# Kernel tuning notes

Hardware: AMD Instinct MI355X
Metric: run time of the kernel (lower is better)

Reference implementation:

```python
import jax, jax.numpy as jnp
import numpy as np

B, H, W, C = 16, 56, 56, 256
NH, WS, SS = 8, 7, 3            # heads, window size, shift size
N = WS * WS                     # tokens per window (49)
NW = (H // WS) * (W // WS)      # windows per image (64)
HID = 4 * C                     # mlp hidden
SCALE = (C // NH) ** -0.5
EPS = 1e-5


def _rel_pos_index():
    coords = np.stack(np.meshgrid(np.arange(WS), np.arange(WS), indexing='ij'))  # (2,WS,WS)
    cf = coords.reshape(2, -1)
    rel = (cf[:, :, None] - cf[:, None, :]).transpose(1, 2, 0).copy()  # (N,N,2)
    rel[:, :, 0] += WS - 1
    rel[:, :, 1] += WS - 1
    rel[:, :, 0] *= 2 * WS - 1
    return rel.sum(-1).reshape(-1)  # (N*N,)

REL_IDX = jnp.asarray(_rel_pos_index())


def _attn_mask():
    # Swin SW-MSA mask for the cyclic shift
    img = np.zeros((H, W), np.float32)
    cnt = 0
    for hs in (slice(0, -WS), slice(-WS, -SS), slice(-SS, None)):
        for ws_ in (slice(0, -WS), slice(-WS, -SS), slice(-SS, None)):
            img[hs, ws_] = cnt
            cnt += 1
    mw = img.reshape(H // WS, WS, W // WS, WS).transpose(0, 2, 1, 3).reshape(-1, N)
    am = mw[:, None, :] - mw[:, :, None]
    return np.where(am != 0, -100.0, 0.0).astype(np.float32)  # (NW,N,N)


def layernorm(x, g, b):
    mu = x.mean(-1, keepdims=True)
    var = jnp.mean((x - mu) ** 2, axis=-1, keepdims=True)
    return (x - mu) * jax.lax.rsqrt(var + EPS) * g + b


def window_partition(x):  # (B,H,W,C) -> (B*NW,N,C)
    b = x.shape[0]
    x = x.reshape(b, H // WS, WS, W // WS, WS, C).transpose(0, 1, 3, 2, 4, 5)
    return x.reshape(-1, N, C)


def window_reverse(w):  # (B*NW,N,C) -> (B,H,W,C)
    x = w.reshape(-1, H // WS, W // WS, WS, WS, C).transpose(0, 1, 3, 2, 4, 5)
    return x.reshape(-1, H, W, C)


def setup_inputs() -> dict:
    key = jax.random.key(0)
    ks = jax.random.split(key, 16)
    sd = 0.02
    return {
        'x': jax.random.normal(ks[0], (B, H * W, C), jnp.float32),
        'w_qkv': jax.random.normal(ks[1], (C, 3 * C), jnp.float32) * sd,
        'b_qkv': jnp.zeros((3 * C,), jnp.float32),
        'rel_bias': jax.random.normal(ks[2], ((2 * WS - 1) ** 2, NH), jnp.float32) * sd,
        'w_proj': jax.random.normal(ks[3], (C, C), jnp.float32) * sd,
        'b_proj': jnp.zeros((C,), jnp.float32),
        'g1': jnp.ones((C,), jnp.float32),
        'beta1': jnp.zeros((C,), jnp.float32),
        'g2': jnp.ones((C,), jnp.float32),
        'beta2': jnp.zeros((C,), jnp.float32),
        'w_fc1': jax.random.normal(ks[4], (C, HID), jnp.float32) * sd,
        'b_fc1': jnp.zeros((HID,), jnp.float32),
        'w_fc2': jax.random.normal(ks[5], (HID, C), jnp.float32) * sd,
        'b_fc2': jnp.zeros((C,), jnp.float32),
        'attn_mask': jnp.asarray(_attn_mask()),
    }


def reference(x, w_qkv, b_qkv, rel_bias, w_proj, b_proj, g1, beta1, g2, beta2,
              w_fc1, b_fc1, w_fc2, b_fc2, attn_mask):
    shortcut = x
    xn = layernorm(x, g1, beta1).reshape(B, H, W, C)
    # cyclic shift (shift_size > 0 path)
    xs = jnp.roll(xn, shift=(-SS, -SS), axis=(1, 2))
    xw = window_partition(xs)                                   # (B*NW, N, C)
    qkv = (xw @ w_qkv + b_qkv).reshape(-1, N, 3, NH, C // NH)
    q, k, v = [jnp.transpose(qkv[:, :, i], (0, 2, 1, 3)) for i in range(3)]  # (Bw,NH,N,hd)
    attn = jnp.einsum('whnd,whmd->whnm', q * SCALE, k)          # (Bw,NH,N,N)
    rpb = rel_bias[REL_IDX].reshape(N, N, NH).transpose(2, 0, 1)  # (NH,N,N)
    attn = attn + rpb[None]
    attn = attn.reshape(B, NW, NH, N, N) + attn_mask[None, :, None]
    attn = jax.nn.softmax(attn.reshape(-1, NH, N, N), axis=-1)
    out = jnp.einsum('whnm,whmd->whnd', attn, v)                # (Bw,NH,N,hd)
    out = out.transpose(0, 2, 1, 3).reshape(-1, N, C)
    out = out @ w_proj + b_proj
    xs = window_reverse(out)                                    # (B,H,W,C)
    xr = jnp.roll(xs, shift=(SS, SS), axis=(1, 2)).reshape(B, H * W, C)
    x = shortcut + xr
    h = layernorm(x, g2, beta2)
    h = jax.nn.gelu(h @ w_fc1 + b_fc1, approximate=False) @ w_fc2 + b_fc2
    return x + h
```

## Files before the change

kernel.cpp:

```cpp
#include <hip/hip_runtime.h>
#include <hip/hip_bf16.h>

typedef unsigned short u16;
typedef __bf16 bf16x8 __attribute__((ext_vector_type(8)));
typedef float f32x4 __attribute__((ext_vector_type(4)));
typedef unsigned int u32x4 __attribute__((ext_vector_type(4)));

#define SCALE_F 0.17677669529663687f

__device__ __forceinline__ u16 f2b(float f) {
    unsigned u = __builtin_bit_cast(unsigned, f);
    u = (u + 0x7fffu + ((u >> 16) & 1u)) >> 16;
    return (u16)u;
}

__device__ __forceinline__ f32x4 mfma16(bf16x8 a, bf16x8 b, f32x4 c) {
    return __builtin_amdgcn_mfma_f32_16x16x32_bf16(a, b, c, 0, 0, 0);
}

__global__ __launch_bounds__(256)
void prep_kernel(const float* __restrict__ wqkv, const float* __restrict__ wproj,
                 const float* __restrict__ wfc1, const float* __restrict__ wfc2,
                 const float* __restrict__ relb, const float* __restrict__ amask,
                 u16* __restrict__ wqkvT, u16* __restrict__ wprojT,
                 u16* __restrict__ wfc1T, u16* __restrict__ wfc2T,
                 float* __restrict__ bm)
{
    int idx = blockIdx.x * 256 + threadIdx.x;
    if (idx < 196608) { int n = idx >> 8, k = idx & 255; wqkvT[idx] = f2b(wqkv[k*768 + n]); return; }
    idx -= 196608;
    if (idx < 65536)  { int n = idx >> 8, k = idx & 255; wprojT[idx] = f2b(wproj[k*256 + n]); return; }
    idx -= 65536;
    if (idx < 262144) { int n = idx >> 8, k = idx & 255; wfc1T[idx] = f2b(wfc1[k*1024 + n]); return; }
    idx -= 262144;
    if (idx < 262144) { int n = idx >> 10, k = idx & 1023; wfc2T[idx] = f2b(wfc2[k*256 + n]); return; }
    idx -= 262144;
    int m = idx & 63, t = idx >> 6;
    int n = t & 63; t >>= 6;
    int h = t & 7;  t >>= 3;
    float v = -1e30f;
    if (n < 49 && m < 49) {
        int iq = n / 7, jq = n - iq * 7, ik = m / 7, jk = m - ik * 7;
        int rel = (iq - ik + 6) * 13 + (jq - jk + 6);
        v = relb[rel * 8 + h] + amask[(t * 49 + n) * 49 + m];
    }
    bm[idx] = v;
}

__global__ __launch_bounds__(256)
void ln_kernel(const float* __restrict__ x, const float* __restrict__ g,
               const float* __restrict__ be, u16* __restrict__ out, const int mode)
{
    const int wid  = ((blockIdx.x << 8) + threadIdx.x) >> 6;
    const int lane = threadIdx.x & 63;
    size_t srcoff;
    if (mode == 0) {
        int bw = wid / 49, nt = wid - bw * 49;
        int b = bw >> 6, widx = bw & 63;
        int wh = widx >> 3, ww = widx & 7;
        int ti = nt / 7, tj = nt - ti * 7;
        int hh = wh * 7 + ti + 3; if (hh >= 56) hh -= 56;
        int wp = ww * 7 + tj + 3; if (wp >= 56) wp -= 56;
        srcoff = ((size_t)b * 3136 + hh * 56 + wp) << 8;
    } else {
        srcoff = (size_t)wid << 8;
    }
    float4 v = *(const float4*)(x + srcoff + (lane << 2));
    float s  = v.x + v.y + v.z + v.w;
    float s2 = fmaf(v.x, v.x, fmaf(v.y, v.y, fmaf(v.z, v.z, v.w * v.w)));
    #pragma unroll
    for (int k = 1; k < 64; k <<= 1) { s += __shfl_xor(s, k); s2 += __shfl_xor(s2, k); }
    const float mu   = s * 0.00390625f;
    const float rstd = rsqrtf(s2 * 0.00390625f - mu * mu + 1e-5f);
    float4 gv = *(const float4*)(g  + (lane << 2));
    float4 bv = *(const float4*)(be + (lane << 2));
    ushort4 o;
    o.x = f2b((v.x - mu) * rstd * gv.x + bv.x);
    o.y = f2b((v.y - mu) * rstd * gv.y + bv.y);
    o.z = f2b((v.z - mu) * rstd * gv.z + bv.z);
    o.w = f2b((v.w - mu) * rstd * gv.w + bv.w);
    *(ushort4*)(out + ((size_t)wid << 8) + (lane << 2)) = o;
}

template<int MODE>
__global__ __launch_bounds__(256)
void gemm128(const u16* __restrict__ A, const u16* __restrict__ Bt,
             const float* __restrict__ bias, void* __restrict__ Cout,
             const int N, const int K, const float* __restrict__ resid)
{
    constexpr int LDA = 40;
    __shared__ __align__(16) u16 As[128 * LDA];
    __shared__ __align__(16) u16 Bs[128 * LDA];

    const int tid  = threadIdx.x;
    const int wave = tid >> 6, lane = tid & 63;
    const int q = lane >> 4, l15 = lane & 15;
    const int wm = wave >> 1, wn = wave & 1;
    const int m0 = blockIdx.y << 7, n0 = blockIdx.x << 7;

    f32x4 acc[4][4] = {};

    const int ar = tid >> 2;
    const int ac = (tid & 3) << 3;
    const u16* Ag = A  + (size_t)(m0 + ar) * K + ac;
    const u16* Bg = Bt + (size_t)(n0 + ar) * K + ac;
    const size_t rstep = (size_t)64 * K;

    u32x4 ra0 = *(const u32x4*)Ag;
    u32x4 ra1 = *(const u32x4*)(Ag + rstep);
    u32x4 rb0 = *(const u32x4*)Bg;
    u32x4 rb1 = *(const u32x4*)(Bg + rstep);

    const int KT = K >> 5;
    for (int kt = 0; kt < KT; ++kt) {
        __syncthreads();
        *(u32x4*)&As[ar * LDA + ac]        = ra0;
        *(u32x4*)&As[(ar + 64) * LDA + ac] = ra1;
        *(u32x4*)&Bs[ar * LDA + ac]        = rb0;
        *(u32x4*)&Bs[(ar + 64) * LDA + ac] = rb1;
        if (kt + 1 < KT) {
            const u16* Ag2 = Ag + (kt + 1) * 32;
            const u16* Bg2 = Bg + (kt + 1) * 32;
            ra0 = *(const u32x4*)Ag2;
            ra1 = *(const u32x4*)(Ag2 + rstep);
            rb0 = *(const u32x4*)Bg2;
            rb1 = *(const u32x4*)(Bg2 + rstep);
        }
        __syncthreads();
        bf16x8 af[4], bfv[4];
        #pragma unroll
        for (int i = 0; i < 4; ++i)
            af[i] = *(const bf16x8*)&As[(wm * 64 + i * 16 + l15) * LDA + q * 8];
        #pragma unroll
        for (int j = 0; j < 4; ++j)
            bfv[j] = *(const bf16x8*)&Bs[(wn * 64 + j * 16 + l15) * LDA + q * 8];
        #pragma unroll
        for (int i = 0; i < 4; ++i)
            #pragma unroll
            for (int j = 0; j < 4; ++j)
                acc[i][j] = mfma16(af[i], bfv[j], acc[i][j]);
    }

    #pragma unroll
    for (int i = 0; i < 4; ++i) {
        #pragma unroll
        for (int r = 0; r < 4; ++r) {
            const int m = m0 + wm * 64 + i * 16 + q * 4 + r;
            size_t dstrow = 0;
            if (MODE == 1) {
                int bw = m / 49, nt = m - bw * 49;
                int b = bw >> 6, widx = bw & 63;
                int wh = widx >> 3, ww2 = widx & 7;
                int ti = nt / 7, tj = nt - ti * 7;
                int hh = wh * 7 + ti + 3;  if (hh >= 56) hh -= 56;
                int wp = ww2 * 7 + tj + 3; if (wp >= 56) wp -= 56;
                dstrow = ((size_t)b * 3136 + hh * 56 + wp) << 8;
            }
            #pragma unroll
            for (int j = 0; j < 4; ++j) {
                const int col = n0 + wn * 64 + j * 16 + l15;
                float v = acc[i][j][r] + bias[col];
                if (MODE == 0) {
                    ((u16*)Cout)[(size_t)m * N + col] = f2b(v);
                } else if (MODE == 2) {
                    float y = 0.7978845608028654f * (v + 0.044715f * v * v * v);
                    float t = __expf(2.0f * y);
                    float rr = __builtin_amdgcn_rcpf(t + 1.0f);
                    v = v - v * rr;
                    ((u16*)Cout)[(size_t)m * N + col] = f2b(v);
                } else if (MODE == 3) {
                    const size_t o = (size_t)m * N + col;
                    ((float*)Cout)[o] = resid[o] + v;
                } else {
                    const size_t o = dstrow + col;
                    ((float*)Cout)[o] = resid[o] + v;
                }
            }
        }
    }
}

__global__ __launch_bounds__(64)
void attn_kernel(const u16* __restrict__ qkv, const float* __restrict__ bm,
                 u16* __restrict__ out)
{
    constexpr int LDP = 72;
    __shared__ __align__(16) u16 Pl[64 * LDP];
    __shared__ __align__(16) u16 Vt[32 * LDP];

    const int bw   = blockIdx.x >> 3;
    const int h    = blockIdx.x & 7;
    const int widx = bw & 63;
    const int lane = threadIdx.x;
    const int q = lane >> 4, l15 = lane & 15;

    const u16* base = qkv + (size_t)bw * 49 * 768 + h * 32;

    {
        const int key = lane;
        const u16* vp = base + 512 + (size_t)(key < 49 ? key : 0) * 768;
        __align__(16) u16 tmp[32];
        #pragma unroll
        for (int c = 0; c < 4; ++c)
            *(u32x4*)&tmp[c * 8] = *(const u32x4*)(vp + c * 8);
        #pragma unroll
        for (int d = 0; d < 32; ++d)
            Vt[d * LDP + key] = (key < 49) ? tmp[d] : (u16)0;
    }

    bf16x8 aq[4], bk[4];
    #pragma unroll
    for (int i = 0; i < 4; ++i) {
        int row = i * 16 + l15; row = (row < 49) ? row : 0;
        aq[i] = *(const bf16x8*)(base + (size_t)row * 768 + q * 8);
    }
    #pragma unroll
    for (int j = 0; j < 4; ++j) {
        int key = j * 16 + l15; key = (key < 49) ? key : 0;
        bk[j] = *(const bf16x8*)(base + (size_t)key * 768 + 256 + q * 8);
    }
    f32x4 s[4][4];
    #pragma unroll
    for (int i = 0; i < 4; ++i)
        #pragma unroll
        for (int j = 0; j < 4; ++j) {
            f32x4 z = {0.f, 0.f, 0.f, 0.f};
            s[i][j] = mfma16(aq[i], bk[j], z);
        }

    const float* bmb = bm + ((size_t)(widx * 8 + h) << 12);
    #pragma unroll
    for (int i = 0; i < 4; ++i) {
        #pragma unroll
        for (int r = 0; r < 4; ++r) {
            const int n = i * 16 + q * 4 + r;
            const float* rowp = bmb + (n << 6) + l15;
            #pragma unroll
            for (int j = 0; j < 4; ++j)
                s[i][j][r] = fmaf(s[i][j][r], SCALE_F, rowp[j * 16]);
        }
    }

    #pragma unroll
    for (int i = 0; i < 4; ++i) {
        #pragma unroll
        for (int r = 0; r < 4; ++r) {
            float mx = fmaxf(fmaxf(s[i][0][r], s[i][1][r]), fmaxf(s[i][2][r], s[i][3][r]));
            #pragma unroll
            for (int k = 1; k < 16; k <<= 1) mx = fmaxf(mx, __shfl_xor(mx, k));
            float p[4], sum = 0.f;
            #pragma unroll
            for (int j = 0; j < 4; ++j) { p[j] = __expf(s[i][j][r] - mx); sum += p[j]; }
            #pragma unroll
            for (int k = 1; k < 16; k <<= 1) sum += __shfl_xor(sum, k);
            const float inv = 1.0f / sum;
            const int n = i * 16 + q * 4 + r;
            #pragma unroll
            for (int j = 0; j < 4; ++j)
                Pl[n * LDP + j * 16 + l15] = f2b(p[j] * inv);
        }
    }
    __syncthreads();

    f32x4 o[4][2] = {};
    #pragma unroll
    for (int ks = 0; ks < 2; ++ks) {
        bf16x8 ap[4], bv[2];
        #pragma unroll
        for (int i = 0; i < 4; ++i)
            ap[i] = *(const bf16x8*)&Pl[(i * 16 + l15) * LDP + ks * 32 + q * 8];
        #pragma unroll
        for (int jd = 0; jd < 2; ++jd)
            bv[jd] = *(const bf16x8*)&Vt[(jd * 16 + l15) * LDP + ks * 32 + q * 8];
        #pragma unroll
        for (int i = 0; i < 4; ++i)
            #pragma unroll
            for (int jd = 0; jd < 2; ++jd)
                o[i][jd] = mfma16(ap[i], bv[jd], o[i][jd]);
    }

    #pragma unroll
    for (int i = 0; i < 4; ++i) {
        #pragma unroll
        for (int r = 0; r < 4; ++r) {
            const int n = i * 16 + q * 4 + r;
            if (n < 49) {
                u16* op = out + ((size_t)(bw * 49 + n) << 8) + h * 32;
                #pragma unroll
                for (int jd = 0; jd < 2; ++jd)
                    op[jd * 16 + l15] = f2b(o[i][jd][r]);
            }
        }
    }
}

extern "C" void kernel_launch(void* const* d_in, const int* in_sizes, int n_in,
                              void* d_out, int out_size, void* d_ws, size_t ws_size,
                              hipStream_t stream) {
    const float* x      = (const float*)d_in[0];
    const float* w_qkv  = (const float*)d_in[1];
    const float* b_qkv  = (const float*)d_in[2];
    const float* rel_b  = (const float*)d_in[3];
    const float* w_proj = (const float*)d_in[4];
    const float* b_proj = (const float*)d_in[5];
    const float* g1     = (const float*)d_in[6];
    const float* be1    = (const float*)d_in[7];
    const float* g2     = (const float*)d_in[8];
    const float* be2    = (const float*)d_in[9];
    const float* w_fc1  = (const float*)d_in[10];
    const float* b_fc1  = (const float*)d_in[11];
    const float* w_fc2  = (const float*)d_in[12];
    const float* b_fc2  = (const float*)d_in[13];
    const float* amask  = (const float*)d_in[14];

    char* ws = (char*)d_ws;
    u16*   xw     = (u16*)(ws);
    u16*   qkvb   = (u16*)(ws + 25690112);
    u16*   attno  = (u16*)(ws + 102760448);
    float* x2     = (float*)(ws + 128450560);
    u16*   wqkvT  = (u16*)(ws + 179830784);
    u16*   wprojT = (u16*)(ws + 180224000);
    u16*   wfc1T  = (u16*)(ws + 180355072);
    u16*   wfc2T  = (u16*)(ws + 180879360);
    float* bm     = (float*)(ws + 181403648);
    u16*   h1     = qkvb;

    prep_kernel<<<12288, 256, 0, stream>>>(w_qkv, w_proj, w_fc1, w_fc2, rel_b, amask,
                                           wqkvT, wprojT, wfc1T, wfc2T, bm);
    ln_kernel<<<12544, 256, 0, stream>>>(x, g1, be1, xw, 0);
    gemm128<0><<<dim3(6, 392), 256, 0, stream>>>(xw, wqkvT, b_qkv, qkvb, 768, 256, nullptr);
    attn_kernel<<<8192, 64, 0, stream>>>(qkvb, bm, attno);
    gemm128<1><<<dim3(2, 392), 256, 0, stream>>>(attno, wprojT, b_proj, x2, 256, 256, x);
    ln_kernel<<<12544, 256, 0, stream>>>(x2, g2, be2, xw, 1);
    gemm128<2><<<dim3(8, 392), 256, 0, stream>>>(xw, wfc1T, b_fc1, h1, 1024, 256, nullptr);
    gemm128<3><<<dim3(2, 392), 256, 0, stream>>>(h1, wfc2T, b_fc2, (float*)d_out, 256, 1024, x2);
}
```

Baseline: 375.4 us.

## Store residual intermediate in bf16 and remap GEMM blocks for XCD locality

The post-attention residual x2 is now stored as bf16 rather than fp32. It is written by the proj GEMM, read by the second layernorm and read as the residual in the fc2 GEMM, which halves that traffic. GEMM launches switch to a 1D grid whose block index is remapped so that consecutive row blocks land on the same XCD, aiming to improve L2 reuse of A tiles across column blocks. The trade-off is bf16 rounding in the residual stream, which adds accuracy error.

```diff
diff --git a/kernel.cpp b/kernel.cpp
--- a/kernel.cpp
+++ b/kernel.cpp
@@ -12,6 +12,10 @@
     unsigned u = __builtin_bit_cast(unsigned, f);
     u = (u + 0x7fffu + ((u >> 16) & 1u)) >> 16;
     return (u16)u;
+}
+__device__ __forceinline__ float b2f(u16 b) {
+    unsigned u = ((unsigned)b) << 16;
+    return __builtin_bit_cast(float, u);
 }
 
 __device__ __forceinline__ f32x4 mfma16(bf16x8 a, bf16x8 b, f32x4 c) {
@@ -48,12 +52,13 @@
 }
 
 __global__ __launch_bounds__(256)
-void ln_kernel(const float* __restrict__ x, const float* __restrict__ g,
-               const float* __restrict__ be, u16* __restrict__ out, const int mode)
+void ln_kernel(const float* __restrict__ x, const u16* __restrict__ xb,
+               const float* __restrict__ g, const float* __restrict__ be,
+               u16* __restrict__ out, const int mode)
 {
     const int wid  = ((blockIdx.x << 8) + threadIdx.x) >> 6;
     const int lane = threadIdx.x & 63;
-    size_t srcoff;
+    float4 v;
     if (mode == 0) {
         int bw = wid / 49, nt = wid - bw * 49;
         int b = bw >> 6, widx = bw & 63;
@@ -61,11 +66,12 @@
         int ti = nt / 7, tj = nt - ti * 7;
         int hh = wh * 7 + ti + 3; if (hh >= 56) hh -= 56;
         int wp = ww * 7 + tj + 3; if (wp >= 56) wp -= 56;
-        srcoff = ((size_t)b * 3136 + hh * 56 + wp) << 8;
+        size_t srcoff = ((size_t)b * 3136 + hh * 56 + wp) << 8;
+        v = *(const float4*)(x + srcoff + (lane << 2));
     } else {
-        srcoff = (size_t)wid << 8;
-    }
-    float4 v = *(const float4*)(x + srcoff + (lane << 2));
+        ushort4 raw = *(const ushort4*)(xb + ((size_t)wid << 8) + (lane << 2));
+        v.x = b2f(raw.x); v.y = b2f(raw.y); v.z = b2f(raw.z); v.w = b2f(raw.w);
+    }
     float s  = v.x + v.y + v.z + v.w;
     float s2 = fmaf(v.x, v.x, fmaf(v.y, v.y, fmaf(v.z, v.z, v.w * v.w)));
     #pragma unroll
@@ -86,7 +92,8 @@
 __global__ __launch_bounds__(256)
 void gemm128(const u16* __restrict__ A, const u16* __restrict__ Bt,
              const float* __restrict__ bias, void* __restrict__ Cout,
-             const int N, const int K, const float* __restrict__ resid)
+             const int N, const int K, const void* __restrict__ resid,
+             const int NB)
 {
     constexpr int LDA = 40;
     __shared__ __align__(16) u16 As[128 * LDA];
@@ -96,7 +103,13 @@
     const int wave = tid >> 6, lane = tid & 63;
     const int q = lane >> 4, l15 = lane & 15;
     const int wm = wave >> 1, wn = wave & 1;
-    const int m0 = blockIdx.y << 7, n0 = blockIdx.x << 7;
+
+    const int bid  = blockIdx.x;
+    const int xcd  = bid & 7;
+    const int t    = bid >> 3;
+    const int colb = t % NB;
+    const int rowb = xcd + ((t / NB) << 3);
+    const int m0 = rowb << 7, n0 = colb << 7;
 
     f32x4 acc[4][4] = {};
 
@@ -164,16 +177,16 @@
                     ((u16*)Cout)[(size_t)m * N + col] = f2b(v);
                 } else if (MODE == 2) {
                     float y = 0.7978845608028654f * (v + 0.044715f * v * v * v);
-                    float t = __expf(2.0f * y);
-                    float rr = __builtin_amdgcn_rcpf(t + 1.0f);
+                    float tt = __expf(2.0f * y);
+                    float rr = __builtin_amdgcn_rcpf(tt + 1.0f);
                     v = v - v * rr;
                     ((u16*)Cout)[(size_t)m * N + col] = f2b(v);
                 } else if (MODE == 3) {
                     const size_t o = (size_t)m * N + col;
-                    ((float*)Cout)[o] = resid[o] + v;
+                    ((float*)Cout)[o] = b2f(((const u16*)resid)[o]) + v;
                 } else {
                     const size_t o = dstrow + col;
-                    ((float*)Cout)[o] = resid[o] + v;
+                    ((u16*)Cout)[o] = f2b(((const float*)resid)[o] + v);
                 }
             }
         }
@@ -317,21 +330,21 @@
     u16*   xw     = (u16*)(ws);
     u16*   qkvb   = (u16*)(ws + 25690112);
     u16*   attno  = (u16*)(ws + 102760448);
-    float* x2     = (float*)(ws + 128450560);
-    u16*   wqkvT  = (u16*)(ws + 179830784);
-    u16*   wprojT = (u16*)(ws + 180224000);
-    u16*   wfc1T  = (u16*)(ws + 180355072);
-    u16*   wfc2T  = (u16*)(ws + 180879360);
-    float* bm     = (float*)(ws + 181403648);
+    u16*   x2b    = (u16*)(ws + 128450560);
+    u16*   wqkvT  = (u16*)(ws + 154140672);
+    u16*   wprojT = (u16*)(ws + 154533888);
+    u16*   wfc1T  = (u16*)(ws + 154664960);
+    u16*   wfc2T  = (u16*)(ws + 155189248);
+    float* bm     = (float*)(ws + 155713536);
     u16*   h1     = qkvb;
 
     prep_kernel<<<12288, 256, 0, stream>>>(w_qkv, w_proj, w_fc1, w_fc2, rel_b, amask,
                                            wqkvT, wprojT, wfc1T, wfc2T, bm);
-    ln_kernel<<<12544, 256, 0, stream>>>(x, g1, be1, xw, 0);
-    gemm128<0><<<dim3(6, 392), 256, 0, stream>>>(xw, wqkvT, b_qkv, qkvb, 768, 256, nullptr);
+    ln_kernel<<<12544, 256, 0, stream>>>(x, nullptr, g1, be1, xw, 0);
+    gemm128<0><<<392 * 6, 256, 0, stream>>>(xw, wqkvT, b_qkv, qkvb, 768, 256, nullptr, 6);
     attn_kernel<<<8192, 64, 0, stream>>>(qkvb, bm, attno);
-    gemm128<1><<<dim3(2, 392), 256, 0, stream>>>(attno, wprojT, b_proj, x2, 256, 256, x);
-    ln_kernel<<<12544, 256, 0, stream>>>(x2, g2, be2, xw, 1);
-    gemm128<2><<<dim3(8, 392), 256, 0, stream>>>(xw, wfc1T, b_fc1, h1, 1024, 256, nullptr);
-    gemm128<3><<<dim3(2, 392), 256, 0, stream>>>(h1, wfc2T, b_fc2, (float*)d_out, 256, 1024, x2);
-}
+    gemm128<1><<<392 * 2, 256, 0, stream>>>(attno, wprojT, b_proj, x2b, 256, 256, x, 2);
+    ln_kernel<<<12544, 256, 0, stream>>>(nullptr, x2b, g2, be2, xw, 2);
+    gemm128<2><<<392 * 8, 256, 0, stream>>>(xw, wfc1T, b_fc1, h1, 1024, 256, nullptr, 8);
+    gemm128<3><<<392 * 2, 256, 0, stream>>>(h1, wfc2T, b_fc2, (float*)d_out, 256, 1024, x2b, 2);
+}
```

Result: faster. 348.4 us (-7.2%).
